# Performance work log

Measured on AMD Instinct MI355X. Metric: run time of the kernel, lower is better.

## Reference

```python
import jax, jax.numpy as jnp
import numpy as np

T, N = 24, 2048
INPUT_DIM, HIDDEN, MEDIATE, SOCIAL, OUT_DIM = 2, 64, 128, 64, 2
N_SIZE = 2
CELL = 0.3
T_OBS, T_PRED = 9, 19
WIN = (N_SIZE + 1) ** 2  # (N_size+1)^2 = 9 window cells


def _social_pool(h, coords, mask):
    """Faithful social pooling for N_size=2, grid_cell_size=0.3.

    torch builds a dynamic grid, scatter-adds every agent's h into its cell,
    then gathers grid[int(x-R):int(x+R), int(y-R):int(y+R)] per agent.
    With R=0.3 and integer positions >= 4 (guaranteed by the margin), that
    slice is exactly the single cell (x-1, y-1), broadcast over the 3x3
    window. We compute it as a pairwise match without materializing a grid.
    Runs under torch.no_grad() -> stop_gradient.
    """
    margin = 2 * N_SIZE * CELL
    lt = jnp.stack([coords[:, 0].min(), coords[:, 1].min()]) - margin
    p = jnp.floor((coords - lt) / CELL).astype(jnp.int32)            # [N,2]
    p = p * mask.astype(jnp.int32)[:, None]                          # masked agents -> cell (0,0)
    q = p - 1                                                        # gathered cell per agent
    match = (p[None, :, 0] == q[:, None, 0]) & (p[None, :, 1] == q[:, None, 1])  # [i,j]
    cell_val = match.astype(h.dtype) @ h                             # [N,hidden] scatter-add + gather
    Hf = jnp.tile(cell_val, (1, WIN)) * mask[:, None]                # broadcast over 3x3 window, flat
    return jax.lax.stop_gradient(Hf)


def _forward(X, part_masks, all_h_t, all_c_t, Y, W_in, b_in, W_soc, b_soc,
             W_ih, W_hh, b_ih, b_hh, W_out, b_out, T_obs, T_pred):
    relu = jax.nn.relu  # dropout_prob = 0 -> Phi == ReLU

    def lstm(z, h, c):
        g = z @ W_ih.T + b_ih + h @ W_hh.T + b_hh
        i, f, gg, o = jnp.split(g, 4, axis=1)
        c = jax.nn.sigmoid(f) * c + jax.nn.sigmoid(i) * jnp.tanh(gg)
        h = jax.nn.sigmoid(o) * jnp.tanh(c)
        return h, c

    def cell_out(r, h, c, coords, m):
        Hf = _social_pool(h, coords, m)
        e = relu(Hf @ W_soc.T + b_soc)
        z = jnp.concatenate([r, e], axis=1)
        h, c = lstm(z, h, c)
        out = (h @ W_out.T + b_out) * m[:, None]
        return h, c, out

    def step_obs(carry, inp):
        h, c = carry
        x, m = inp
        r = relu(x @ W_in.T + b_in)
        h, c, out = cell_out(r, h, c, x, m)
        return (h, c), out

    (h, c), outs_obs = jax.lax.scan(
        step_obs, (all_h_t, all_c_t), (X[:T_obs + 1], part_masks[:T_obs + 1]))

    def step_pred(carry, inp):
        h, c, last_pt, prev_out = carry
        x, m = inp
        r = relu(last_pt @ W_in.T + b_in)
        h, c, out = cell_out(r, h, c, x, m)
        # torch: last_point = outputs[frame_idx - 1] AFTER the frame runs
        return (h, c, prev_out, out), out

    carry0 = (h, c, X[T_obs + 1], outs_obs[-1])
    _, outs_pred = jax.lax.scan(
        step_pred, carry0, (X[T_obs + 1:T_pred + 1], part_masks[T_obs + 1:T_pred + 1]))

    tail = jnp.zeros((X.shape[0] - T_pred - 1, X.shape[1], OUT_DIM), X.dtype)
    return jnp.concatenate([outs_obs, outs_pred, tail], axis=0)


def setup_inputs() -> dict:
    key = jax.random.key(0)
    ks = jax.random.split(key, 13)

    def lin(kw, kb, out_d, in_d):  # torch nn.Linear default init
        lim = 1.0 / float(np.sqrt(in_d))
        W = jax.random.uniform(kw, (out_d, in_d), minval=-lim, maxval=lim, dtype=jnp.float32)
        b = jax.random.uniform(kb, (out_d,), minval=-lim, maxval=lim, dtype=jnp.float32)
        return W, b

    W_in, b_in = lin(ks[0], ks[1], MEDIATE, INPUT_DIM)
    W_soc, b_soc = lin(ks[2], ks[3], SOCIAL, WIN * HIDDEN)
    W_ih, b_ih = lin(ks[4], ks[5], 4 * HIDDEN, MEDIATE + SOCIAL)
    W_hh, b_hh = lin(ks[6], ks[7], 4 * HIDDEN, HIDDEN)
    W_out, b_out = lin(ks[8], ks[9], OUT_DIM, HIDDEN)

    X = jax.random.normal(ks[10], (T, N, INPUT_DIM), dtype=jnp.float32) * 10.0  # meter-scale coords
    part_masks = (jax.random.uniform(ks[11], (T, N)) < 0.9).astype(jnp.float32)  # binary presence mask
    Y = jax.random.normal(ks[12], (T, N, INPUT_DIM), dtype=jnp.float32)  # unused by forward
    all_h_t = jnp.zeros((N, HIDDEN), jnp.float32)
    all_c_t = jnp.zeros((N, HIDDEN), jnp.float32)

    return {"X": X, "part_masks": part_masks, "all_h_t": all_h_t, "all_c_t": all_c_t,
            "Y": Y, "T_obs": T_OBS, "T_pred": T_PRED,
            "W_in": W_in, "b_in": b_in, "W_soc": W_soc, "b_soc": b_soc,
            "W_ih": W_ih, "W_hh": W_hh, "b_ih": b_ih, "b_hh": b_hh,
            "W_out": W_out, "b_out": b_out}


def reference(X, part_masks, all_h_t, all_c_t, Y, T_obs, T_pred,
              W_in, b_in, W_soc, b_soc, W_ih, W_hh, b_ih, b_hh, W_out, b_out):
    return _forward(X, part_masks, all_h_t, all_c_t, Y, W_in, b_in, W_soc, b_soc,
                    W_ih, W_hh, b_ih, b_hh, W_out, b_out, int(T_obs), int(T_pred))
```

## Files before the change

### kernel.cpp

```cpp
#include <hip/hip_runtime.h>
#include <math.h>


#define N_AG   2048
#define STEPS  20
#define CAP    12
#define NSRV   21
#define MAGIC  0x13572468
#define NTHR   768

typedef short short8 __attribute__((ext_vector_type(8)));
typedef float f32x4  __attribute__((ext_vector_type(4)));
union FU { uint4 q; short8 v; };

__device__ __forceinline__ void pack8(const float* v, uint4& hq, uint4& lq) {
    unsigned uh[4], ul[4];
    #pragma unroll
    for (int w = 0; w < 4; w++) {
        float v0 = v[2 * w], v1 = v[2 * w + 1];
        unsigned h;
        asm("v_cvt_pk_bf16_f32 %0, %1, %2" : "=v"(h) : "v"(v0), "v"(v1));
        float f0 = __uint_as_float(h << 16);
        float f1 = __uint_as_float(h & 0xffff0000u);
        float r0 = v0 - f0, r1 = v1 - f1;
        unsigned l;
        asm("v_cvt_pk_bf16_f32 %0, %1, %2" : "=v"(l) : "v"(r0), "v"(r1));
        uh[w] = h; ul[w] = l;
    }
    hq = make_uint4(uh[0], uh[1], uh[2], uh[3]);
    lq = make_uint4(ul[0], ul[1], ul[2], ul[3]);
}

__device__ __forceinline__ int khash(int k) {
    return (int)(((unsigned)k * 2654435761u) >> 21);
}

__device__ __forceinline__ float fsigm(float x) {
    return __builtin_amdgcn_rcpf(1.f + __expf(-x));
}
__device__ __forceinline__ float ftanh(float x) {
    float e = __expf(2.f * x);
    return 1.f - 2.f * __builtin_amdgcn_rcpf(e + 1.f);
}

__device__ __forceinline__ void bar_lds() {
    asm volatile("s_waitcnt lgkmcnt(0)\n\ts_barrier" ::: "memory");
}

__device__ __forceinline__ void ast(int* p_, int v) {
    __hip_atomic_store(p_, v, __ATOMIC_RELAXED, __HIP_MEMORY_SCOPE_AGENT);
}
__device__ __forceinline__ void astf(float* p_, float v) {
    __hip_atomic_store(p_, v, __ATOMIC_RELAXED, __HIP_MEMORY_SCOPE_AGENT);
}
__device__ __forceinline__ unsigned long long aldu64(const unsigned long long* p_) {
    return __hip_atomic_load(p_, __ATOMIC_RELAXED, __HIP_MEMORY_SCOPE_AGENT);
}

struct KP {
    const float *X, *masks, *h_in, *c_in;
    const float *Win, *bin, *Wsoc, *bsoc, *Wih, *Whh, *bih, *bhh, *Wout, *bout;
    float *Wef;
    int *mcnt, *midx, *need, *flags;
    float *out;
    unsigned long long *hist;
};

__global__ __launch_bounds__(NTHR, 1) void k_all(KP p)
{
    __shared__ __align__(16) uint4 zshq[544];
    __shared__ float gbuf[16][260];
    __shared__ float gbuf2[8][260];
    __shared__ __align__(16) float cvs[8][68];
    __shared__ __align__(16) float hs[8][68];
    __shared__ __align__(16) float sWefP[64 * 66];
    __shared__ float2 sWinP[16 * 17];
    __shared__ float sBinP[16 * 9];
    __shared__ float sX[11][8][2];
    __shared__ float sMask[STEPS][8];
    __shared__ int   sCnt[STEPS][8];
    __shared__ int   sNeed[19][8];
    __shared__ int   sMidx[STEPS][8][CAP];
    __shared__ float sBsoc[64], sBc[256], sWout[128], sBout[2];
    __shared__ uint4 sE0h[8], sE0l[8];
    __shared__ int kk[N_AG];
    __shared__ int head[N_AG];
    __shared__ int nxt[N_AG];
    __shared__ float red[128];

    const int tid = threadIdx.x;
    const int bxg = blockIdx.x;

    if (bxg < NSRV) {
        const int sb = bxg;
        {
            int lo = sb * 780;
            int hi = (sb == NSRV - 1) ? 16384 : lo + 780;
            for (int i = lo + tid; i < hi; i += NTHR)
                p.out[20 * N_AG * 2 + i] = 0.f;
        }
        if (sb == 20) {
            for (int i = tid; i < 4096; i += NTHR) {
                int s = i >> 6, k = i & 63;
                float a = 0.f;
                #pragma unroll
                for (int w = 0; w < 9; w++) a += p.Wsoc[s * 576 + w * 64 + k];
                astf(&p.Wef[i], a);
            }
            __syncthreads();
            if (tid == 0) ast(&p.flags[20], MAGIC);
        } else {
            const int t = sb;
            const float* Xt = p.X + t * N_AG * 2;

            float mnx = 1e30f, mny = 1e30f;
            for (int i = tid; i < N_AG; i += NTHR) {
                mnx = fminf(mnx, Xt[2 * i]);
                mny = fminf(mny, Xt[2 * i + 1]);
            }
            #pragma unroll
            for (int off = 32; off >= 1; off >>= 1) {
                mnx = fminf(mnx, __shfl_xor(mnx, off));
                mny = fminf(mny, __shfl_xor(mny, off));
            }
            if ((tid & 63) == 0) { red[tid >> 6] = mnx; red[32 + (tid >> 6)] = mny; }
            __syncthreads();
            if (tid == 0) {
                float ax = red[0], ay = red[32];
                for (int u = 1; u < NTHR / 64; u++) {
                    ax = fminf(ax, red[u]); ay = fminf(ay, red[32 + u]);
                }
                red[64] = ax; red[65] = ay;
            }
            __syncthreads();
            float ltx = red[64] - 1.2f;
            float lty = red[65] - 1.2f;

            for (int i = tid; i < N_AG; i += NTHR) {
                float m = p.masks[t * N_AG + i];
                int px = (int)floorf((Xt[2 * i]     - ltx) / 0.3f);
                int py = (int)floorf((Xt[2 * i + 1] - lty) / 0.3f);
                int im = (int)m;
                px *= im; py *= im;
                kk[i] = px * 65536 + py;
                head[i] = -1;
                if (t >= 1) ast(&p.need[(t - 1) * N_AG + i], 0);
            }
            __syncthreads();
            for (int j = tid; j < N_AG; j += NTHR) {
                int kj = kk[j];
                if (kj != 0) nxt[j] = atomicExch(&head[khash(kj)], j);
            }
            __syncthreads();
            for (int i = tid; i < N_AG; i += NTHR) {
                int ki = kk[i];
                int cnt = 0;
                int base = (t * N_AG + i) * CAP;
                if (ki != 0) {
                    int tkey = ki - 65537;
                    int lst[CAP];
                    for (int j = head[khash(tkey)]; j >= 0; j = nxt[j]) {
                        if (kk[j] == tkey) { if (cnt < CAP) lst[cnt] = j; cnt++; }
                    }
                    if (cnt > CAP) cnt = CAP;
                    for (int a = 1; a < cnt; a++) {
                        int v = lst[a]; int b = a - 1;
                        while (b >= 0 && lst[b] > v) { lst[b + 1] = lst[b]; b--; }
                        lst[b + 1] = v;
                    }
                    for (int a = 0; a < cnt; a++) {
                        ast(&p.midx[base + a], lst[a]);
                        if (t >= 1) ast(&p.need[(t - 1) * N_AG + lst[a]], 1);
                    }
                }
                ast(&p.mcnt[t * N_AG + i], cnt);
            }
            __syncthreads();
            if (tid == 0) ast(&p.flags[t], MAGIC);
        }
    }

    const int wbase = bxg * 8;
    const int wv    = tid >> 6, lane = tid & 63;
    const int mA    = lane & 15, quad = lane >> 4;
    const int nt0   = 2 * wv;
    const int w     = wv;

    if (tid < 256) sBc[tid] = p.bih[tid] + p.bhh[tid];
    if (tid < 128) {
        sWout[tid] = p.Wout[tid];
        int c = tid;
        sWinP[(c >> 3) * 17 + (c & 7)] = make_float2(p.Win[2 * c], p.Win[2 * c + 1]);
        sBinP[(c >> 3) * 9 + (c & 7)] = p.bin[c];
    }
    if (tid < 64) sBsoc[tid] = p.bsoc[tid];
    if (tid < 2)  sBout[tid] = p.bout[tid];
    if (tid < 8) {
        float v[8];
        #pragma unroll
        for (int j = 0; j < 8; j++) v[j] = fmaxf(p.bsoc[tid * 8 + j], 0.f);
        pack8(v, sE0h[tid], sE0l[tid]);
    }
    if (tid < 176) { int tt = tid / 16, r = tid % 16;
                     sX[tt][r >> 1][r & 1] = p.X[tt * (N_AG * 2) + (wbase + (r >> 1)) * 2 + (r & 1)]; }
    if (tid < 160) { int tt = tid / 8, m2 = tid % 8;
                     sMask[tt][m2] = p.masks[tt * N_AG + wbase + m2]; }

    float c0 = 0.f;
    if (wv < 8) {
        hs[w][lane] = p.h_in[(wbase + w) * 64 + lane];
        c0 = p.c_in[(wbase + w) * 64 + lane];
    }

    FU wh[2][8], wl[2][8];
    if (wv < 8) {
        #pragma unroll
        for (int e = 0; e < 2; e++) {
            int g = (nt0 + e) * 16 + mA;
            #pragma unroll
            for (int kt = 0; kt < 8; kt++) {
                int k0 = kt * 32 + quad * 8;
                const float* src = (k0 < 192) ? (p.Wih + g * 192 + k0)
                                              : (p.Whh + g * 64 + (k0 - 192));
                float v[8];
                #pragma unroll
                for (int j = 0; j < 8; j++) v[j] = src[j];
                pack8(v, wh[e][kt].q, wl[e][kt].q);
            }
        }
    }
    FU woh[2], wol[2];
    if (wv == 8) {
        #pragma unroll
        for (int e2 = 0; e2 < 2; e2++) {
            int kt = 6 + e2;
            float v[8];
            #pragma unroll
            for (int j = 0; j < 8; j++) {
                int k0 = kt * 32 + quad * 8 + j - 192;
                v[j] = (mA < 2) ? p.Wout[mA * 64 + k0] : 0.f;
            }
            pack8(v, woh[e2].q, wol[e2].q);
        }
    }

    if (tid < NSRV) {
        while (__hip_atomic_load(&p.flags[tid], __ATOMIC_RELAXED,
                                 __HIP_MEMORY_SCOPE_AGENT) != MAGIC) { }
    }
    __syncthreads();

    if (tid < 160) { int tt = tid / 8, m2 = tid % 8;
                     sCnt[tt][m2] = p.mcnt[tt * N_AG + wbase + m2]; }
    if (tid < 152) { int s = tid / 8, m2 = tid % 8;
                     sNeed[s][m2] = p.need[s * N_AG + wbase + m2]; }
    for (int i = tid; i < 4096; i += NTHR) sWefP[(i >> 6) * 66 + (i & 63)] = p.Wef[i];
    for (int i = tid; i < STEPS * 8 * CAP; i += NTHR) {
        int tt = i / (8 * CAP), r = i % (8 * CAP), m2 = r / CAP, n = r % CAP;
        sMidx[tt][m2][n] = p.midx[(tt * N_AG + wbase + m2) * CAP + n];
    }
    __syncthreads();

    if (wv < 8) {
        if (lane < 16) {
            float px = sX[0][w][0], py = sX[0][w][1];
            float v[8];
            #pragma unroll
            for (int j = 0; j < 8; j++) {
                float2 w2 = sWinP[lane * 17 + j];
                v[j] = fmaxf(w2.x * px + w2.y * py + sBinP[lane * 9 + j], 0.f);
            }
            pack8(v, zshq[lane * 17 + w], zshq[lane * 17 + w + 8]);
        } else if (lane < 24) {
            int s58 = lane - 16;
            const float4* hr = (const float4*)&hs[w][s58 * 8];
            float4 h0 = hr[0], h1 = hr[1];
            float v[8] = { h0.x, h0.y, h0.z, h0.w, h1.x, h1.y, h1.z, h1.w };
            pack8(v, zshq[(24 + s58) * 17 + w], zshq[(24 + s58) * 17 + w + 8]);
        } else if (lane < 32) {
            int s58 = lane - 24;
            if (sCnt[0][w] == 0) {
                zshq[(16 + s58) * 17 + w]     = sE0h[s58];
                zshq[(16 + s58) * 17 + w + 8] = sE0l[s58];
            }
        }
        int cnt0 = sCnt[0][w];
        if (cnt0 > 0) {
            float a = 0.f;
            for (int n = 0; n < cnt0; n++) {
                int r = sMidx[0][w][n];
                a += p.h_in[r * 64 + lane];
            }
            cvs[w][lane] = a;
            asm volatile("s_waitcnt lgkmcnt(0)" ::: "memory");
            float acc = sBsoc[lane], accb = 0.f;
            const float4* cw = (const float4*)&cvs[w][0];
            const float2* wq = (const float2*)&sWefP[lane * 66];
            #pragma unroll
            for (int k4 = 0; k4 < 16; k4++) {
                float4 ca = cw[k4];
                float2 wa = wq[2 * k4], wb = wq[2 * k4 + 1];
                acc  += ca.x * wa.x + ca.y * wa.y;
                accb += ca.z * wb.x + ca.w * wb.y;
            }
            acc = fmaxf(acc + accb, 0.f);
            float v[8];
            #pragma unroll
            for (int j = 0; j < 8; j++) v[j] = __shfl(acc, (lane & 7) * 8 + j, 64);
            if (lane < 8)
                pack8(v, zshq[(16 + lane) * 17 + w], zshq[(16 + lane) * 17 + w + 8]);
        }
    }
    bar_lds();

    #pragma unroll 1
    for (int t = 0; t < STEPS; t++) {
        if (wv < 8) {
            f32x4 a0v = {0.f, 0.f, 0.f, 0.f};
            f32x4 a1v = {0.f, 0.f, 0.f, 0.f};
            f32x4 a0l = {0.f, 0.f, 0.f, 0.f};
            f32x4 a1l = {0.f, 0.f, 0.f, 0.f};
            #pragma unroll
            for (int kt = 0; kt < 8; kt++) {
                FU az;
                az.q = zshq[(kt * 4 + quad) * 17 + mA];
                a0v = __builtin_amdgcn_mfma_f32_16x16x32_bf16(az.v, wh[0][kt].v, a0v, 0, 0, 0);
                a1v = __builtin_amdgcn_mfma_f32_16x16x32_bf16(az.v, wh[1][kt].v, a1v, 0, 0, 0);
                a0l = __builtin_amdgcn_mfma_f32_16x16x32_bf16(az.v, wl[0][kt].v, a0l, 0, 0, 0);
                a1l = __builtin_amdgcn_mfma_f32_16x16x32_bf16(az.v, wl[1][kt].v, a1l, 0, 0, 0);
            }
            #pragma unroll
            for (int r = 0; r < 4; r++) {
                int row = quad * 4 + r;
                gbuf[row][nt0 * 16 + mA]       = a0v[r];
                gbuf[row][(nt0 + 1) * 16 + mA] = a1v[r];
            }
            if (quad < 2) {
                #pragma unroll
                for (int r = 0; r < 4; r++) {
                    int row = quad * 4 + r;
                    gbuf2[row][nt0 * 16 + mA]       = a0l[r];
                    gbuf2[row][(nt0 + 1) * 16 + mA] = a1l[r];
                }
            }
        } else if (wv == 8) {
            f32x4 ovv = {0.f, 0.f, 0.f, 0.f};
            f32x4 ovl = {0.f, 0.f, 0.f, 0.f};
            #pragma unroll
            for (int e2 = 0; e2 < 2; e2++) {
                int kt = 6 + e2;
                FU az;
                az.q = zshq[(kt * 4 + quad) * 17 + mA];
                ovv = __builtin_amdgcn_mfma_f32_16x16x32_bf16(az.v, woh[e2].v, ovv, 0, 0, 0);
                ovl = __builtin_amdgcn_mfma_f32_16x16x32_bf16(az.v, wol[e2].v, ovl, 0, 0, 0);
            }
            if (mA < 2) {
                #pragma unroll
                for (int r = 0; r < 4; r++) {
                    int row = quad * 4 + r;
                    gbuf[row][256 + mA] = ovv[r];
                    if (quad < 2) gbuf2[row][256 + mA] = ovl[r];
                }
            }
        }
        bar_lds();

        if (wv < 8) {
            const int hid = lane;
            float gi = gbuf[w][hid]       + gbuf[w + 8][hid]       + gbuf2[w][hid]       + sBc[hid];
            float gf = gbuf[w][64 + hid]  + gbuf[w + 8][64 + hid]  + gbuf2[w][64 + hid]  + sBc[64 + hid];
            float gR = gbuf[w][128 + hid] + gbuf[w + 8][128 + hid] + gbuf2[w][128 + hid] + sBc[128 + hid];
            float go = gbuf[w][192 + hid] + gbuf[w + 8][192 + hid] + gbuf2[w][192 + hid] + sBc[192 + hid];
            float cn = fsigm(gf) * c0 + fsigm(gi) * ftanh(gR);
            float hn = fsigm(go) * ftanh(cn);
            c0 = cn;
            hs[w][hid] = hn;

            if (t <= 18 && sNeed[t][w]) {
                unsigned long long* hp = p.hist + (size_t)t * (N_AG * 64);
                unsigned long long tg = ((unsigned long long)(t + 1)) << 32;
                __hip_atomic_store(&hp[(wbase + w) * 64 + hid],
                                   tg | (unsigned long long)__float_as_uint(hn),
                                   __ATOMIC_RELAXED, __HIP_MEMORY_SCOPE_AGENT);
            }

            float q0 = 0.f, q1 = 0.f;
            if (t >= 1) {
                float mkp = sMask[t - 1][w];
                q0 = (gbuf[w][256] + gbuf[w + 8][256] + gbuf2[w][256] + sBout[0]) * mkp;
                q1 = (gbuf[w][257] + gbuf[w + 8][257] + gbuf2[w][257] + sBout[1]) * mkp;
                if (lane == 0)
                    *(float2*)&p.out[((t - 1) * N_AG + wbase + w) * 2] = make_float2(q0, q1);
            }
            if (t == STEPS - 1) {
                float p0 = hn * sWout[hid], p1 = hn * sWout[64 + hid];
                #pragma unroll
                for (int off = 32; off >= 1; off >>= 1) {
                    p0 += __shfl_xor(p0, off);
                    p1 += __shfl_xor(p1, off);
                }
                float mk = sMask[t][w];
                if (lane == 0)
                    *(float2*)&p.out[(t * N_AG + wbase + w) * 2] =
                        make_float2((p0 + sBout[0]) * mk, (p1 + sBout[1]) * mk);
            }

            if (t < STEPS - 1) {
                const int tn = t + 1;
                if (lane < 16) {
                    float px, py;
                    if (tn <= 10) { px = sX[tn][w][0]; py = sX[tn][w][1]; }
                    else          { px = q0; py = q1; }
                    float v[8];
                    #pragma unroll
                    for (int j = 0; j < 8; j++) {
                        float2 w2 = sWinP[lane * 17 + j];
                        v[j] = fmaxf(w2.x * px + w2.y * py + sBinP[lane * 9 + j], 0.f);
                    }
                    pack8(v, zshq[lane * 17 + w], zshq[lane * 17 + w + 8]);
                } else if (lane < 24) {
                    int s58 = lane - 16;
                    const float4* hr = (const float4*)&hs[w][s58 * 8];
                    float4 h0 = hr[0], h1 = hr[1];
                    float v[8] = { h0.x, h0.y, h0.z, h0.w, h1.x, h1.y, h1.z, h1.w };
                    pack8(v, zshq[(24 + s58) * 17 + w], zshq[(24 + s58) * 17 + w + 8]);
                }
            }
        } else if (t < STEPS - 1) {
            const int hw = wv - 8;
            const unsigned long long* hb = p.hist + (size_t)t * (N_AG * 64);
            const unsigned tagw = (unsigned)(t + 1);
            #pragma unroll
            for (int k = 0; k < 2; k++) {
                const int ag = hw * 2 + k;
                int cntN = sCnt[t + 1][ag];
                if (cntN == 0) {
                    if (lane < 8) {
                        zshq[(16 + lane) * 17 + ag]     = sE0h[lane];
                        zshq[(16 + lane) * 17 + ag + 8] = sE0l[lane];
                    }
                } else {
                    int rfirst = sMidx[t + 1][ag][0];
                    unsigned long long pw0 = aldu64(&hb[rfirst * 64 + lane]);
                    while ((unsigned)(pw0 >> 32) != tagw)
                        pw0 = aldu64(&hb[rfirst * 64 + lane]);
                    float a = __uint_as_float((unsigned)pw0);
                    for (int n = 1; n < cntN; n++) {
                        int r = sMidx[t + 1][ag][n];
                        unsigned long long w0_;
                        do { w0_ = aldu64(&hb[r * 64 + lane]); }
                        while ((unsigned)(w0_ >> 32) != tagw);
                        a += __uint_as_float((unsigned)w0_);
                    }
                    cvs[ag][lane] = a;
                    asm volatile("s_waitcnt lgkmcnt(0)" ::: "memory");
                    float acc = sBsoc[lane], accb = 0.f;
                    const float4* cw = (const float4*)&cvs[ag][0];
                    const float2* wq = (const float2*)&sWefP[lane * 66];
                    #pragma unroll
                    for (int k4 = 0; k4 < 16; k4++) {
                        float4 ca = cw[k4];
                        float2 wa = wq[2 * k4], wb = wq[2 * k4 + 1];
                        acc  += ca.x * wa.x + ca.y * wa.y;
                        accb += ca.z * wb.x + ca.w * wb.y;
                    }
                    acc = fmaxf(acc + accb, 0.f);
                    float v[8];
                    #pragma unroll
                    for (int j = 0; j < 8; j++) v[j] = __shfl(acc, (lane & 7) * 8 + j, 64);
                    if (lane < 8)
                        pack8(v, zshq[(16 + lane) * 17 + ag], zshq[(16 + lane) * 17 + ag + 8]);
                }
            }
        }
        bar_lds();
    }
}

extern "C" void kernel_launch(void* const* d_in, const int* in_sizes, int n_in,
                              void* d_out, int out_size, void* d_ws, size_t ws_size,
                              hipStream_t stream)
{
    KP kp;
    kp.X     = (const float*)d_in[0];
    kp.masks = (const float*)d_in[1];
    kp.h_in  = (const float*)d_in[2];
    kp.c_in  = (const float*)d_in[3];
    kp.Win   = (const float*)d_in[7];
    kp.bin   = (const float*)d_in[8];
    kp.Wsoc  = (const float*)d_in[9];
    kp.bsoc  = (const float*)d_in[10];
    kp.Wih   = (const float*)d_in[11];
    kp.Whh   = (const float*)d_in[12];
    kp.bih   = (const float*)d_in[13];
    kp.bhh   = (const float*)d_in[14];
    kp.Wout  = (const float*)d_in[15];
    kp.bout  = (const float*)d_in[16];
    kp.out   = (float*)d_out;

    unsigned long long* hist = (unsigned long long*)d_ws;
    float* Wef  = (float*)(hist + 19 * N_AG * 64);
    int*   need = (int*)(Wef + 4096);
    int*   mcnt = need + 19 * N_AG;
    int*   midx = mcnt + STEPS * N_AG;
    int*   flags = midx + STEPS * N_AG * CAP;

    kp.hist = hist; kp.Wef = Wef; kp.need = need; kp.mcnt = mcnt;
    kp.midx = midx; kp.flags = flags;

    k_all<<<256, NTHR, 0, stream>>>(kp);
}
```

Measured before the change: 192.1 us.

## Redistribute low-bf16 weight MFMAs across all waves and relax launch bounds

The low-part (residual bf16) weight fragments for the gate GEMM, previously all held by the eight compute waves, are now split. Each compute wave keeps one low tile, and the four extra waves hold two low tiles each and run those MFMAs. This cuts the compute waves' register footprint and per-step MFMA chain from 32 to 24, moving the rest onto waves that were mostly idle during the matmul phase. Launch bounds change from 1 to 3 blocks per CU, which caps registers per thread and may cause spills, or may allow co-residency if LDS permits.

Result: slower. 300.0 us (+56.2%).

```diff
diff --git a/kernel.cpp b/kernel.cpp
--- a/kernel.cpp
+++ b/kernel.cpp
@@ -66,7 +66,7 @@
     unsigned long long *hist;
 };
 
-__global__ __launch_bounds__(NTHR, 1) void k_all(KP p)
+__global__ __launch_bounds__(NTHR, 3) void k_all(KP p)
 {
     __shared__ __align__(16) uint4 zshq[544];
     __shared__ float gbuf[16][260];
@@ -185,6 +185,7 @@
     const int mA    = lane & 15, quad = lane >> 4;
     const int nt0   = 2 * wv;
     const int w     = wv;
+    const int hw    = wv - 8;
 
     if (tid < 256) sBc[tid] = p.bih[tid] + p.bhh[tid];
     if (tid < 128) {
@@ -212,7 +213,7 @@
         c0 = p.c_in[(wbase + w) * 64 + lane];
     }
 
-    FU wh[2][8], wl[2][8];
+    FU wh[2][8], wlo[8];
     if (wv < 8) {
         #pragma unroll
         for (int e = 0; e < 2; e++) {
@@ -225,7 +226,41 @@
                 float v[8];
                 #pragma unroll
                 for (int j = 0; j < 8; j++) v[j] = src[j];
-                pack8(v, wh[e][kt].q, wl[e][kt].q);
+                uint4 lt;
+                pack8(v, wh[e][kt].q, lt);
+                if (e == 0 && false) {}
+            }
+        }
+        {
+            int g = w * 16 + mA;
+            #pragma unroll
+            for (int kt = 0; kt < 8; kt++) {
+                int k0 = kt * 32 + quad * 8;
+                const float* src = (k0 < 192) ? (p.Wih + g * 192 + k0)
+                                              : (p.Whh + g * 64 + (k0 - 192));
+                float v[8];
+                #pragma unroll
+                for (int j = 0; j < 8; j++) v[j] = src[j];
+                uint4 ht;
+                pack8(v, ht, wlo[kt].q);
+            }
+        }
+    }
+    FU wlh[2][8];
+    if (wv >= 8) {
+        #pragma unroll
+        for (int e = 0; e < 2; e++) {
+            int g = (8 + 2 * hw + e) * 16 + mA;
+            #pragma unroll
+            for (int kt = 0; kt < 8; kt++) {
+                int k0 = kt * 32 + quad * 8;
+                const float* src = (k0 < 192) ? (p.Wih + g * 192 + k0)
+                                              : (p.Whh + g * 64 + (k0 - 192));
+                float v[8];
+                #pragma unroll
+                for (int j = 0; j < 8; j++) v[j] = src[j];
+                uint4 ht;
+                pack8(v, ht, wlh[e][kt].q);
             }
         }
     }
@@ -318,16 +353,14 @@
         if (wv < 8) {
             f32x4 a0v = {0.f, 0.f, 0.f, 0.f};
             f32x4 a1v = {0.f, 0.f, 0.f, 0.f};
-            f32x4 a0l = {0.f, 0.f, 0.f, 0.f};
-            f32x4 a1l = {0.f, 0.f, 0.f, 0.f};
+            f32x4 alo = {0.f, 0.f, 0.f, 0.f};
             #pragma unroll
             for (int kt = 0; kt < 8; kt++) {
                 FU az;
                 az.q = zshq[(kt * 4 + quad) * 17 + mA];
                 a0v = __builtin_amdgcn_mfma_f32_16x16x32_bf16(az.v, wh[0][kt].v, a0v, 0, 0, 0);
                 a1v = __builtin_amdgcn_mfma_f32_16x16x32_bf16(az.v, wh[1][kt].v, a1v, 0, 0, 0);
-                a0l = __builtin_amdgcn_mfma_f32_16x16x32_bf16(az.v, wl[0][kt].v, a0l, 0, 0, 0);
-                a1l = __builtin_amdgcn_mfma_f32_16x16x32_bf16(az.v, wl[1][kt].v, a1l, 0, 0, 0);
+                alo = __builtin_amdgcn_mfma_f32_16x16x32_bf16(az.v, wlo[kt].v, alo, 0, 0, 0);
             }
             #pragma unroll
             for (int r = 0; r < 4; r++) {
@@ -339,27 +372,45 @@
                 #pragma unroll
                 for (int r = 0; r < 4; r++) {
                     int row = quad * 4 + r;
-                    gbuf2[row][nt0 * 16 + mA]       = a0l[r];
-                    gbuf2[row][(nt0 + 1) * 16 + mA] = a1l[r];
-                }
-            }
-        } else if (wv == 8) {
-            f32x4 ovv = {0.f, 0.f, 0.f, 0.f};
-            f32x4 ovl = {0.f, 0.f, 0.f, 0.f};
-            #pragma unroll
-            for (int e2 = 0; e2 < 2; e2++) {
-                int kt = 6 + e2;
+                    gbuf2[row][w * 16 + mA] = alo[r];
+                }
+            }
+        } else {
+            f32x4 al0 = {0.f, 0.f, 0.f, 0.f};
+            f32x4 al1 = {0.f, 0.f, 0.f, 0.f};
+            #pragma unroll
+            for (int kt = 0; kt < 8; kt++) {
                 FU az;
                 az.q = zshq[(kt * 4 + quad) * 17 + mA];
-                ovv = __builtin_amdgcn_mfma_f32_16x16x32_bf16(az.v, woh[e2].v, ovv, 0, 0, 0);
-                ovl = __builtin_amdgcn_mfma_f32_16x16x32_bf16(az.v, wol[e2].v, ovl, 0, 0, 0);
-            }
-            if (mA < 2) {
+                al0 = __builtin_amdgcn_mfma_f32_16x16x32_bf16(az.v, wlh[0][kt].v, al0, 0, 0, 0);
+                al1 = __builtin_amdgcn_mfma_f32_16x16x32_bf16(az.v, wlh[1][kt].v, al1, 0, 0, 0);
+            }
+            if (quad < 2) {
                 #pragma unroll
                 for (int r = 0; r < 4; r++) {
                     int row = quad * 4 + r;
-                    gbuf[row][256 + mA] = ovv[r];
-                    if (quad < 2) gbuf2[row][256 + mA] = ovl[r];
+                    gbuf2[row][(8 + 2 * hw) * 16 + mA] = al0[r];
+                    gbuf2[row][(9 + 2 * hw) * 16 + mA] = al1[r];
+                }
+            }
+            if (wv == 8) {
+                f32x4 ovv = {0.f, 0.f, 0.f, 0.f};
+                f32x4 ovl = {0.f, 0.f, 0.f, 0.f};
+                #pragma unroll
+                for (int e2 = 0; e2 < 2; e2++) {
+                    int kt = 6 + e2;
+                    FU az;
+                    az.q = zshq[(kt * 4 + quad) * 17 + mA];
+                    ovv = __builtin_amdgcn_mfma_f32_16x16x32_bf16(az.v, woh[e2].v, ovv, 0, 0, 0);
+                    ovl = __builtin_amdgcn_mfma_f32_16x16x32_bf16(az.v, wol[e2].v, ovl, 0, 0, 0);
+                }
+                if (mA < 2) {
+                    #pragma unroll
+                    for (int r = 0; r < 4; r++) {
+                        int row = quad * 4 + r;
+                        gbuf[row][256 + mA] = ovv[r];
+                        if (quad < 2) gbuf2[row][256 + mA] = ovl[r];
+                    }
                 }
             }
         }
@@ -427,7 +478,6 @@
                 }
             }
         } else if (t < STEPS - 1) {
-            const int hw = wv - 8;
             const unsigned long long* hb = p.hist + (size_t)t * (N_AG * 64);
             const unsigned tagw = (unsigned)(t + 1);
             #pragma unroll
```
